# Performance work log

Hardware: AMD Instinct MI355X
Metric: run time of the kernel (lower is better)

## Reference

```python
import jax, jax.numpy as jnp
import numpy as np

N_NODES = 100000
N_EDGES = 1600000
IN_FEATS = 128
OUT_FEATS = 128


def setup_inputs() -> dict:
    key = jax.random.key(0)
    k1, k2, k3, k4, k5 = jax.random.split(key, 5)
    feat = jax.random.normal(k1, (N_NODES, IN_FEATS), dtype=jnp.float32)
    # He (kaiming) uniform-ish init scale for the weights
    bound = np.sqrt(6.0 / IN_FEATS).astype(np.float32)
    weight_u = jax.random.uniform(k2, (IN_FEATS, OUT_FEATS), jnp.float32, -bound, bound)
    weight_v = jax.random.uniform(k3, (IN_FEATS, OUT_FEATS), jnp.float32, -bound, bound)
    bias = jnp.zeros((OUT_FEATS,), dtype=jnp.float32)
    src = jax.random.randint(k4, (N_EDGES,), 0, N_NODES, dtype=jnp.int32)
    dst = jax.random.randint(k5, (N_EDGES,), 0, N_NODES, dtype=jnp.int32)
    return {"feat": feat, "weight_u": weight_u, "weight_v": weight_v,
            "bias": bias, "src": src, "dst": dst}


def reference(feat, weight_u, weight_v, bias, src, dst):
    n = feat.shape[0]
    # in_feats (128) is not > out_feats (128) -> aggregate first, then matmul
    # m_i = sum_{j in N(i)} h_j  (copy_u + sum over edges)
    agg = jax.ops.segment_sum(feat[src], dst, num_segments=n)  # [N, in_feats]
    rst_u = jnp.matmul(agg, weight_u)                          # [N, out_feats]
    rst_v = jnp.matmul(feat, weight_v)                         # [N, out_feats]
    # in-degree normalization, clamped at 1
    deg = jax.ops.segment_sum(jnp.ones_like(dst, dtype=feat.dtype), dst,
                              num_segments=n)
    norm = 1.0 / jnp.maximum(deg, 1.0)                         # [N]
    out = jax.nn.relu(rst_v + norm[:, None] * rst_u + bias)
    return out
```

## Files before the change

### kernel.cpp

```cpp
#include <hip/hip_runtime.h>
#include <hip/hip_bf16.h>
#include <stdint.h>

#define NN 100000
#define NE 1600000
#define NF 128
#define NTILE ((NN + 63) / 64)
#define GEMM_G 782
#define B_BKT 1563
#define NB2 128
#define EPB (NE / NB2)
#define NCNT (B_BKT * NB2)
#define SC2A ((NCNT + 255) / 256)

typedef __attribute__((ext_vector_type(8))) __bf16 bf16x8;
typedef __attribute__((ext_vector_type(4))) float floatx4;
typedef __attribute__((ext_vector_type(4))) unsigned short ushortx4;
typedef __attribute__((ext_vector_type(8))) unsigned short ushortx8;
typedef __attribute__((ext_vector_type(4))) unsigned int uintx4;

static __device__ __forceinline__ unsigned short f2bf(float x) {
    union { float f; unsigned u; } v; v.f = x;
    unsigned r = v.u + 0x7fffu + ((v.u >> 16) & 1u);
    return (unsigned short)(r >> 16);
}
static __device__ __forceinline__ float bflo(unsigned w) {
    union { unsigned u; float f; } v; v.u = w << 16; return v.f;
}
static __device__ __forceinline__ float bfhi(unsigned w) {
    union { unsigned u; float f; } v; v.u = w & 0xffff0000u; return v.f;
}

__global__ void k_convert(const float* __restrict__ s, unsigned short* __restrict__ d, int n4) {
    int i = blockIdx.x * blockDim.x + threadIdx.x;
    if (i < n4) {
        floatx4 f = __builtin_nontemporal_load((const floatx4*)s + i);
        ushortx4 o;
        o.x = f2bf(f.x); o.y = f2bf(f.y); o.z = f2bf(f.z); o.w = f2bf(f.w);
        __builtin_nontemporal_store(o, (ushortx4*)d + i);
    }
}

__global__ void k_prep(const float* __restrict__ wv, const float* __restrict__ wu,
                       unsigned short* __restrict__ w2t) {
    int id = blockIdx.x * 256 + threadIdx.x;
    if (id >= 128 * 32) return;
    int n = id >> 5, kg = id & 31;
    const float* srcm = (kg < 16) ? wv : wu;
    int k0 = (kg & 15) * 8;
    ushortx8 o;
#pragma unroll
    for (int j = 0; j < 8; ++j)
        o[j] = f2bf(srcm[(k0 + j) * 128 + n]);
    int dchunk = n * 32 + (kg ^ (n & 7));
    *(ushortx8*)(w2t + dchunk * 8) = o;
}

__global__ void k_count(const int* __restrict__ dst, int* __restrict__ counts) {
    __shared__ int h[B_BKT];
    int tid = threadIdx.x;
    for (int i = tid; i < B_BKT; i += 256) h[i] = 0;
    __syncthreads();
    int base = blockIdx.x * EPB, end = base + EPB;
    for (int i = base + tid; i < end; i += 256) {
        int d = __builtin_nontemporal_load(&dst[i]);
        atomicAdd(&h[d >> 6], 1);
    }
    __syncthreads();
    for (int i = tid; i < B_BKT; i += 256)
        counts[i * NB2 + blockIdx.x] = h[i];
}

__global__ void k_scan2_a(int* __restrict__ counts, int* __restrict__ bsums) {
    __shared__ int sh[256];
    int i = blockIdx.x * 256 + threadIdx.x;
    int v = (i < NCNT) ? counts[i] : 0;
    sh[threadIdx.x] = v;
    __syncthreads();
    for (int off = 1; off < 256; off <<= 1) {
        int u = (threadIdx.x >= off) ? sh[threadIdx.x - off] : 0;
        __syncthreads();
        sh[threadIdx.x] += u;
        __syncthreads();
    }
    if (i < NCNT) counts[i] = sh[threadIdx.x] - v;
    if (threadIdx.x == 255) bsums[blockIdx.x] = sh[255];
}
__global__ void k_scan2_b(int* __restrict__ bsums) {
    __shared__ int sh[1024];
    int t = threadIdx.x;
    int v = (t < SC2A) ? bsums[t] : 0;
    sh[t] = v;
    __syncthreads();
    for (int off = 1; off < 1024; off <<= 1) {
        int u = (t >= off) ? sh[t - off] : 0;
        __syncthreads();
        sh[t] += u;
        __syncthreads();
    }
    if (t < SC2A) bsums[t] = sh[t] - v;
}
__global__ void k_scan2_c(int* __restrict__ counts, const int* __restrict__ bsums) {
    int i = blockIdx.x * 256 + threadIdx.x;
    if (i < NCNT) counts[i] += bsums[blockIdx.x];
}

__global__ void k_binscatter(const int* __restrict__ src, const int* __restrict__ dst,
                             const int* __restrict__ counts, unsigned* __restrict__ streams) {
    __shared__ int cur[B_BKT];
    int tid = threadIdx.x;
    for (int i = tid; i < B_BKT; i += 256)
        cur[i] = counts[i * NB2 + blockIdx.x];
    __syncthreads();
    int base = blockIdx.x * EPB, end = base + EPB;
    for (int i = base + tid; i < end; i += 256) {
        int d = __builtin_nontemporal_load(&dst[i]);
        int s = __builtin_nontemporal_load(&src[i]);
        int b = d >> 6;
        unsigned packed = ((unsigned)(d & 63) << 17) | (unsigned)s;
        int pos = atomicAdd(&cur[b], 1);
        streams[pos] = packed;
    }
}

__global__ void k_csr(const unsigned* __restrict__ streams,
                      const int* __restrict__ counts,
                      int* __restrict__ offs, int* __restrict__ csr) {
    __shared__ int hist[64];
    __shared__ int nodeoff[65];
    int tid = threadIdx.x;
    int bkt = blockIdx.x;
    int s = counts[bkt * NB2];
    int e = (bkt == B_BKT - 1) ? NE : counts[(bkt + 1) * NB2];
    if (tid < 64) hist[tid] = 0;
    __syncthreads();
    for (int i = s + tid; i < e; i += 256)
        atomicAdd(&hist[streams[i] >> 17], 1);
    __syncthreads();
    if (tid == 0) {
        int run = 0;
#pragma unroll
        for (int n = 0; n < 64; ++n) { nodeoff[n] = run; run += hist[n]; }
        nodeoff[64] = run;
    }
    __syncthreads();
    if (tid < 64) {
        int node = bkt * 64 + tid;
        if (node < NN) offs[node] = s + nodeoff[tid];
        hist[tid] = nodeoff[tid];
    }
    if (bkt == B_BKT - 1 && tid == 0) offs[NN] = NE;
    __syncthreads();
    for (int i = s + tid; i < e; i += 256) {
        unsigned v = streams[i];
        int p = atomicAdd(&hist[v >> 17], 1);
        csr[s + p] = (int)(v & 0x1FFFFu);
    }
}

__global__ void k_aggregate(const unsigned short* __restrict__ featb,
                            const int* __restrict__ offs,
                            const int* __restrict__ csr,
                            unsigned short* __restrict__ aggb) {
    int lane = threadIdx.x & 63;
    int node = blockIdx.x * 4 + (threadIdx.x >> 6);
    if (node >= NN) return;
    int g = lane >> 4;
    int l16 = lane & 15;
    int s0 = offs[node], s1 = offs[node + 1];
    float acc[8];
#pragma unroll
    for (int j = 0; j < 8; ++j) acc[j] = 0.f;

    int base = s0 + g;
    for (; base + 4 < s1; base += 8) {
        int e0 = __builtin_nontemporal_load(&csr[base]);
        int e1 = __builtin_nontemporal_load(&csr[base + 4]);
        uintx4 w0 = *(const uintx4*)(featb + (e0 << 7) + (l16 << 3));
        uintx4 w1 = *(const uintx4*)(featb + (e1 << 7) + (l16 << 3));
        acc[0] += bflo(w0.x); acc[1] += bfhi(w0.x);
        acc[2] += bflo(w0.y); acc[3] += bfhi(w0.y);
        acc[4] += bflo(w0.z); acc[5] += bfhi(w0.z);
        acc[6] += bflo(w0.w); acc[7] += bfhi(w0.w);
        acc[0] += bflo(w1.x); acc[1] += bfhi(w1.x);
        acc[2] += bflo(w1.y); acc[3] += bfhi(w1.y);
        acc[4] += bflo(w1.z); acc[5] += bfhi(w1.z);
        acc[6] += bflo(w1.w); acc[7] += bfhi(w1.w);
    }
    if (base < s1) {
        int e0 = __builtin_nontemporal_load(&csr[base]);
        uintx4 w0 = *(const uintx4*)(featb + (e0 << 7) + (l16 << 3));
        acc[0] += bflo(w0.x); acc[1] += bfhi(w0.x);
        acc[2] += bflo(w0.y); acc[3] += bfhi(w0.y);
        acc[4] += bflo(w0.z); acc[5] += bfhi(w0.z);
        acc[6] += bflo(w0.w); acc[7] += bfhi(w0.w);
    }
#pragma unroll
    for (int j = 0; j < 8; ++j) {
        acc[j] += __shfl_xor(acc[j], 16, 64);
        acc[j] += __shfl_xor(acc[j], 32, 64);
    }
    if (lane < 16) {
        int dg = s1 - s0; if (dg < 1) dg = 1;
        float scale = 1.0f / (float)dg;
        ushortx8 o;
#pragma unroll
        for (int j = 0; j < 8; ++j) o[j] = f2bf(acc[j] * scale);
        __builtin_nontemporal_store(o, (ushortx8*)(aggb + (size_t)node * NF + (l16 << 3)));
    }
}

static __device__ __forceinline__ void gemm_tile(
    const unsigned short* lds, const bf16x8* a, const float* bsv,
    int rb, int quad, int l15, float* __restrict__ out) {
    floatx4 acc[8];
#pragma unroll
    for (int ct = 0; ct < 8; ++ct) acc[ct] = (floatx4){0.f, 0.f, 0.f, 0.f};
#pragma unroll
    for (int ct = 0; ct < 8; ++ct) {
        int n = ct * 16 + l15;
        int rowoff = n << 8;
        int sw = n & 7;
#pragma unroll
        for (int ks = 0; ks < 8; ++ks) {
            int kg = ks * 4 + quad;
            bf16x8 b = *(const bf16x8*)(&lds[rowoff + ((kg ^ sw) << 3)]);
            acc[ct] = __builtin_amdgcn_mfma_f32_16x16x32_bf16(a[ks], b, acc[ct], 0, 0, 0);
        }
    }
#pragma unroll
    for (int r = 0; r < 4; ++r) {
        int row = rb + quad * 4 + r;
        if (row < NN) {
#pragma unroll
            for (int ct = 0; ct < 8; ++ct) {
                int col = ct * 16 + l15;
                float v = acc[ct][r] + bsv[ct];
                out[(size_t)row * NF + col] = v > 0.f ? v : 0.f;
            }
        }
    }
}

__global__ __launch_bounds__(256, 2) void k_gemm(
    const unsigned short* __restrict__ featb,
    const unsigned short* __restrict__ aggb,
    const unsigned short* __restrict__ w2t,
    const float* __restrict__ bias,
    float* __restrict__ out) {
    __shared__ unsigned short lds[128 * 256];
    for (int i = threadIdx.x; i < 4096; i += 256) {
        ushortx8 w = *(const ushortx8*)(w2t + i * 8);
        *(ushortx8*)(&lds[i * 8]) = w;
    }
    __syncthreads();

    int lane = threadIdx.x & 63;
    int wave = threadIdx.x >> 6;
    int quad = lane >> 4, l15 = lane & 15;

    float bsv[8];
#pragma unroll
    for (int ct = 0; ct < 8; ++ct) bsv[ct] = bias[ct * 16 + l15];

    int t0 = blockIdx.x;
    int t1 = t0 + GEMM_G;
    int t1v = (t1 < NTILE) ? t1 : t0;

    int rb0 = t0 * 64 + wave * 16;
    int rb1 = t1v * 64 + wave * 16;
    int ar0 = rb0 + l15; if (ar0 > NN - 1) ar0 = NN - 1;
    int ar1 = rb1 + l15; if (ar1 > NN - 1) ar1 = NN - 1;
    const unsigned short* fr0 = featb + (size_t)ar0 * NF;
    const unsigned short* ag0 = aggb + (size_t)ar0 * NF;
    const unsigned short* fr1 = featb + (size_t)ar1 * NF;
    const unsigned short* ag1 = aggb + (size_t)ar1 * NF;

    bf16x8 a0[8], a1[8];
#pragma unroll
    for (int ks = 0; ks < 4; ++ks) {
        a0[ks]     = *(const bf16x8*)(fr0 + ks * 32 + quad * 8);
        a0[4 + ks] = *(const bf16x8*)(ag0 + ks * 32 + quad * 8);
    }
#pragma unroll
    for (int ks = 0; ks < 4; ++ks) {
        a1[ks]     = *(const bf16x8*)(fr1 + ks * 32 + quad * 8);
        a1[4 + ks] = *(const bf16x8*)(ag1 + ks * 32 + quad * 8);
    }

    gemm_tile(lds, a0, bsv, rb0, quad, l15, out);
    if (t1 < NTILE)
        gemm_tile(lds, a1, bsv, rb1, quad, l15, out);
}

extern "C" void kernel_launch(void* const* d_in, const int* in_sizes, int n_in,
                              void* d_out, int out_size, void* d_ws, size_t ws_size,
                              hipStream_t stream) {
    const float* feat = (const float*)d_in[0];
    const float* wu   = (const float*)d_in[1];
    const float* wv   = (const float*)d_in[2];
    const float* bias = (const float*)d_in[3];
    const int* src    = (const int*)d_in[4];
    const int* dst    = (const int*)d_in[5];
    float* out        = (float*)d_out;

    char* ws = (char*)d_ws;
    int* counts           = (int*)(ws + 0);
    int* bsums            = (int*)(ws + 800256);
    int* offs             = (int*)(ws + 804352);
    int* csr              = (int*)(ws + 1204480);
    unsigned short* featb = (unsigned short*)(ws + 7604480);
    unsigned short* aggb  = (unsigned short*)(ws + 33204480);
    unsigned short* w2t   = (unsigned short*)(ws + 58804480);
    unsigned* streams     = (unsigned*)aggb;

    k_convert<<<(NN * NF / 4 + 255) / 256, 256, 0, stream>>>(feat, featb, NN * NF / 4);
    k_prep<<<16, 256, 0, stream>>>(wv, wu, w2t);

    k_count<<<NB2, 256, 0, stream>>>(dst, counts);
    k_scan2_a<<<SC2A, 256, 0, stream>>>(counts, bsums);
    k_scan2_b<<<1, 1024, 0, stream>>>(bsums);
    k_scan2_c<<<SC2A, 256, 0, stream>>>(counts, bsums);
    k_binscatter<<<NB2, 256, 0, stream>>>(src, dst, counts, streams);
    k_csr<<<B_BKT, 256, 0, stream>>>(streams, counts, offs, csr);
    k_aggregate<<<(NN + 3) / 4, 256, 0, stream>>>(featb, offs, csr, aggb);
    k_gemm<<<GEMM_G, 256, 0, stream>>>(featb, aggb, w2t, bias, out);
}
```

Before: 317.3 us.

## Fold scan fixup into consumers, widen count/scatter blocks, prefetch gathers in aggregate

Drops the k_scan2_c launch; binscatter and csr now add the block prefix sums inline when they read the counts. The count and binscatter kernels go from 256 to 512 threads per block. The aggregate loop becomes a three-deep software prefetch of gathered feature rows, putting more loads in flight per lane, at the cost of extra registers and per-iteration branches.

```diff
diff --git a/kernel.cpp b/kernel.cpp
--- a/kernel.cpp
+++ b/kernel.cpp
@@ -59,15 +59,15 @@
 __global__ void k_count(const int* __restrict__ dst, int* __restrict__ counts) {
     __shared__ int h[B_BKT];
     int tid = threadIdx.x;
-    for (int i = tid; i < B_BKT; i += 256) h[i] = 0;
+    for (int i = tid; i < B_BKT; i += 512) h[i] = 0;
     __syncthreads();
     int base = blockIdx.x * EPB, end = base + EPB;
-    for (int i = base + tid; i < end; i += 256) {
+    for (int i = base + tid; i < end; i += 512) {
         int d = __builtin_nontemporal_load(&dst[i]);
         atomicAdd(&h[d >> 6], 1);
     }
     __syncthreads();
-    for (int i = tid; i < B_BKT; i += 256)
+    for (int i = tid; i < B_BKT; i += 512)
         counts[i * NB2 + blockIdx.x] = h[i];
 }
 
@@ -100,20 +100,19 @@
     }
     if (t < SC2A) bsums[t] = sh[t] - v;
 }
-__global__ void k_scan2_c(int* __restrict__ counts, const int* __restrict__ bsums) {
-    int i = blockIdx.x * 256 + threadIdx.x;
-    if (i < NCNT) counts[i] += bsums[blockIdx.x];
-}
 
 __global__ void k_binscatter(const int* __restrict__ src, const int* __restrict__ dst,
-                             const int* __restrict__ counts, unsigned* __restrict__ streams) {
+                             const int* __restrict__ counts, const int* __restrict__ bsums,
+                             unsigned* __restrict__ streams) {
     __shared__ int cur[B_BKT];
     int tid = threadIdx.x;
-    for (int i = tid; i < B_BKT; i += 256)
-        cur[i] = counts[i * NB2 + blockIdx.x];
+    for (int i = tid; i < B_BKT; i += 512) {
+        int idx = i * NB2 + blockIdx.x;
+        cur[i] = counts[idx] + bsums[idx >> 8];
+    }
     __syncthreads();
     int base = blockIdx.x * EPB, end = base + EPB;
-    for (int i = base + tid; i < end; i += 256) {
+    for (int i = base + tid; i < end; i += 512) {
         int d = __builtin_nontemporal_load(&dst[i]);
         int s = __builtin_nontemporal_load(&src[i]);
         int b = d >> 6;
@@ -124,14 +123,15 @@
 }
 
 __global__ void k_csr(const unsigned* __restrict__ streams,
-                      const int* __restrict__ counts,
+                      const int* __restrict__ counts, const int* __restrict__ bsums,
                       int* __restrict__ offs, int* __restrict__ csr) {
     __shared__ int hist[64];
     __shared__ int nodeoff[65];
     int tid = threadIdx.x;
     int bkt = blockIdx.x;
-    int s = counts[bkt * NB2];
-    int e = (bkt == B_BKT - 1) ? NE : counts[(bkt + 1) * NB2];
+    int idx = bkt * NB2;
+    int s = counts[idx] + bsums[idx >> 8];
+    int e = (bkt == B_BKT - 1) ? NE : (counts[idx + NB2] + bsums[(idx + NB2) >> 8]);
     if (tid < 64) hist[tid] = 0;
     __syncthreads();
     for (int i = s + tid; i < e; i += 256)
@@ -166,34 +166,40 @@
     int node = blockIdx.x * 4 + (threadIdx.x >> 6);
     if (node >= NN) return;
     int g = lane >> 4;
-    int l16 = lane & 15;
+    int fo = (lane & 15) << 3;
     int s0 = offs[node], s1 = offs[node + 1];
     float acc[8];
 #pragma unroll
     for (int j = 0; j < 8; ++j) acc[j] = 0.f;
 
-    int base = s0 + g;
-    for (; base + 4 < s1; base += 8) {
-        int e0 = __builtin_nontemporal_load(&csr[base]);
-        int e1 = __builtin_nontemporal_load(&csr[base + 4]);
-        uintx4 w0 = *(const uintx4*)(featb + (e0 << 7) + (l16 << 3));
-        uintx4 w1 = *(const uintx4*)(featb + (e1 << 7) + (l16 << 3));
-        acc[0] += bflo(w0.x); acc[1] += bfhi(w0.x);
-        acc[2] += bflo(w0.y); acc[3] += bfhi(w0.y);
-        acc[4] += bflo(w0.z); acc[5] += bfhi(w0.z);
-        acc[6] += bflo(w0.w); acc[7] += bfhi(w0.w);
-        acc[0] += bflo(w1.x); acc[1] += bfhi(w1.x);
-        acc[2] += bflo(w1.y); acc[3] += bfhi(w1.y);
-        acc[4] += bflo(w1.z); acc[5] += bfhi(w1.z);
-        acc[6] += bflo(w1.w); acc[7] += bfhi(w1.w);
-    }
-    if (base < s1) {
-        int e0 = __builtin_nontemporal_load(&csr[base]);
-        uintx4 w0 = *(const uintx4*)(featb + (e0 << 7) + (l16 << 3));
-        acc[0] += bflo(w0.x); acc[1] += bfhi(w0.x);
-        acc[2] += bflo(w0.y); acc[3] += bfhi(w0.y);
-        acc[4] += bflo(w0.z); acc[5] += bfhi(w0.z);
-        acc[6] += bflo(w0.w); acc[7] += bfhi(w0.w);
+    uintx4 w0 = (uintx4){0,0,0,0}, w1 = w0, w2 = w0;
+    int P = s0 + g;
+    if (P < s1) {
+        int c = __builtin_nontemporal_load(&csr[P]);
+        w0 = *(const uintx4*)(featb + ((size_t)c << 7) + fo);
+    }
+    if (P + 4 < s1) {
+        int c = __builtin_nontemporal_load(&csr[P + 4]);
+        w1 = *(const uintx4*)(featb + ((size_t)c << 7) + fo);
+    }
+    if (P + 8 < s1) {
+        int c = __builtin_nontemporal_load(&csr[P + 8]);
+        w2 = *(const uintx4*)(featb + ((size_t)c << 7) + fo);
+    }
+    int Pn = P + 12;
+    for (int pp = s0; pp < s1; pp += 4) {
+        uintx4 cw = w0;
+        w0 = w1; w1 = w2;
+        w2 = (uintx4){0,0,0,0};
+        if (Pn < s1) {
+            int c = __builtin_nontemporal_load(&csr[Pn]);
+            w2 = *(const uintx4*)(featb + ((size_t)c << 7) + fo);
+        }
+        Pn += 4;
+        acc[0] += bflo(cw.x); acc[1] += bfhi(cw.x);
+        acc[2] += bflo(cw.y); acc[3] += bfhi(cw.y);
+        acc[4] += bflo(cw.z); acc[5] += bfhi(cw.z);
+        acc[6] += bflo(cw.w); acc[7] += bfhi(cw.w);
     }
 #pragma unroll
     for (int j = 0; j < 8; ++j) {
@@ -206,7 +212,7 @@
         ushortx8 o;
 #pragma unroll
         for (int j = 0; j < 8; ++j) o[j] = f2bf(acc[j] * scale);
-        __builtin_nontemporal_store(o, (ushortx8*)(aggb + (size_t)node * NF + (l16 << 3)));
+        __builtin_nontemporal_store(o, (ushortx8*)(aggb + (size_t)node * NF + fo));
     }
 }
 
@@ -317,12 +323,11 @@
     k_convert<<<(NN * NF / 4 + 255) / 256, 256, 0, stream>>>(feat, featb, NN * NF / 4);
     k_prep<<<16, 256, 0, stream>>>(wv, wu, w2t);
 
-    k_count<<<NB2, 256, 0, stream>>>(dst, counts);
+    k_count<<<NB2, 512, 0, stream>>>(dst, counts);
     k_scan2_a<<<SC2A, 256, 0, stream>>>(counts, bsums);
     k_scan2_b<<<1, 1024, 0, stream>>>(bsums);
-    k_scan2_c<<<SC2A, 256, 0, stream>>>(counts, bsums);
-    k_binscatter<<<NB2, 256, 0, stream>>>(src, dst, counts, streams);
-    k_csr<<<B_BKT, 256, 0, stream>>>(streams, counts, offs, csr);
+    k_binscatter<<<NB2, 512, 0, stream>>>(src, dst, counts, bsums, streams);
+    k_csr<<<B_BKT, 256, 0, stream>>>(streams, counts, bsums, offs, csr);
     k_aggregate<<<(NN + 3) / 4, 256, 0, stream>>>(featb, offs, csr, aggb);
     k_gemm<<<GEMM_G, 256, 0, stream>>>(featb, aggb, w2t, bias, out);
 }
```

Measured after the change: 310.7 us. 1.02x faster.
